# Optimization experiments

Hardware: AMD Instinct MI355X
Metric: run time of the kernel (lower is better)

Reference implementation:

```python
import jax, jax.numpy as jnp
import numpy as np

EMB_DIM = 2048
N_HEADS = 32
N_KV_HEADS = 8
HEAD_DIM = EMB_DIM // N_HEADS  # 64
N_REP = N_HEADS // N_KV_HEADS  # 4
B = 1
T = 2048


def setup_inputs() -> dict:
    key = jax.random.key(0)
    ks = jax.random.split(key, 7)
    x = jax.random.normal(ks[0], (B, T, EMB_DIM), dtype=jnp.float32)
    # RoPE tables, standard: cos/sin of shape (T, head_dim)
    inv_freq = 1.0 / (10000.0 ** (np.arange(0, HEAD_DIM, 2, dtype=np.float32) / HEAD_DIM))
    pos = np.arange(T, dtype=np.float32)
    ang = pos[:, None] * inv_freq[None, :]            # (T, head_dim/2)
    ang = np.concatenate([ang, ang], axis=-1)         # (T, head_dim)
    cos = jnp.asarray(np.cos(ang), dtype=jnp.float32)
    sin = jnp.asarray(np.sin(ang), dtype=jnp.float32)
    s = 0.02
    Wq = jax.random.normal(ks[1], (EMB_DIM, EMB_DIM), dtype=jnp.float32) * s
    Wk = jax.random.normal(ks[2], (N_KV_HEADS * HEAD_DIM, EMB_DIM), dtype=jnp.float32) * s
    Wv = jax.random.normal(ks[3], (N_KV_HEADS * HEAD_DIM, EMB_DIM), dtype=jnp.float32) * s
    Wo = jax.random.normal(ks[4], (EMB_DIM, EMB_DIM), dtype=jnp.float32) * s
    return {"x": x, "cos": cos, "sin": sin, "Wq": Wq, "Wk": Wk, "Wv": Wv, "Wo": Wo}


def apply_rope(t, cos, sin):
    # t: (b, h, T, d); cos/sin: (T, d)
    d = t.shape[-1]
    x1, x2 = t[..., : d // 2], t[..., d // 2:]
    rotated = jnp.concatenate([-x2, x1], axis=-1)
    return t * cos[None, None] + rotated * sin[None, None]


def reference(x, cos, sin, Wq, Wk, Wv, Wo):
    b, n_tok, _ = x.shape
    q = (x @ Wq.T).reshape(b, n_tok, N_HEADS, HEAD_DIM).transpose(0, 2, 1, 3)
    k = (x @ Wk.T).reshape(b, n_tok, N_KV_HEADS, HEAD_DIM).transpose(0, 2, 1, 3)
    v = (x @ Wv.T).reshape(b, n_tok, N_KV_HEADS, HEAD_DIM).transpose(0, 2, 1, 3)
    q = apply_rope(q, cos, sin)
    k = apply_rope(k, cos, sin)
    # repeat_interleave KV heads to n_heads
    k = jnp.repeat(k, N_REP, axis=1)
    v = jnp.repeat(v, N_REP, axis=1)
    scores = jnp.einsum("bhqd,bhkd->bhqk", q, k) / jnp.sqrt(jnp.float32(HEAD_DIM))
    causal = jnp.tril(jnp.ones((n_tok, n_tok), dtype=bool))
    scores = jnp.where(causal[None, None], scores, -jnp.inf)
    weights = jax.nn.softmax(scores, axis=-1)
    ctx = jnp.einsum("bhqk,bhkd->bhqd", weights, v)
    ctx = ctx.transpose(0, 2, 1, 3).reshape(b, n_tok, EMB_DIM)
    return ctx @ Wo.T
```

## Files before the change

### kernel.cpp

```cpp
#include <hip/hip_runtime.h>
#include <hip/hip_bf16.h>
#include <stdint.h>

#define EMB   2048
#define TOK   2048
#define NH    32
#define NKV   8
#define HD    64
#define QKVN  3072

typedef __attribute__((ext_vector_type(8))) short bf16x8;
typedef __attribute__((ext_vector_type(4))) float f32x4;
typedef __attribute__((ext_vector_type(16))) float f32x16;
typedef __attribute__((ext_vector_type(4))) unsigned int u32x4;

__device__ __forceinline__ void gld16(const void* g, void* l) {
  auto gp = reinterpret_cast<const int __attribute__((address_space(1)))*>(
      reinterpret_cast<uintptr_t>(g));
  auto lp = reinterpret_cast<int __attribute__((address_space(3)))*>(
      reinterpret_cast<uintptr_t>(l));
  __builtin_amdgcn_global_load_lds(gp, lp, 16, 0, 0);
}

__device__ __forceinline__ unsigned int cvtpk_bf16(float lo, float hi) {
  unsigned int r;
  asm("v_cvt_pk_bf16_f32 %0, %1, %2" : "=v"(r) : "v"(lo), "v"(hi));
  return r;
}
__device__ __forceinline__ void pl32swap(unsigned int &a, unsigned int &b) {
  asm volatile("v_permlane32_swap_b32 %0, %1" : "+v"(a), "+v"(b));
}
__device__ __forceinline__ float fexp2(float x) {
  float r;
  asm("v_exp_f32 %0, %1" : "=v"(r) : "v"(x));
  return r;
}

__global__ void cast_all(const float* __restrict__ x,  const float* __restrict__ wq,
                         const float* __restrict__ wk, const float* __restrict__ wv,
                         const float* __restrict__ wo,
                         __hip_bfloat16* __restrict__ xb,
                         __hip_bfloat16* __restrict__ wc,
                         __hip_bfloat16* __restrict__ wob) {
  const size_t M4 = (size_t)4 * 1024 * 1024;
  const size_t M1 = (size_t)1024 * 1024;
  size_t i = ((size_t)blockIdx.x * 256 + threadIdx.x) * 4;
  const float* src;
  __hip_bfloat16* dst;
  if (i < M4)                    { src = x  + i;                 dst = xb  + i; }
  else if (i < 2*M4)             { src = wq + (i - M4);          dst = wc  + (i - M4); }
  else if (i < 2*M4 + M1)        { src = wk + (i - 2*M4);        dst = wc  + M4 + (i - 2*M4); }
  else if (i < 2*M4 + 2*M1)      { src = wv + (i - 2*M4 - M1);   dst = wc  + M4 + M1 + (i - 2*M4 - M1); }
  else                           { src = wo + (i - 2*M4 - 2*M1); dst = wob + (i - 2*M4 - 2*M1); }
  float4 v = *reinterpret_cast<const float4*>(src);
  dst[0] = __float2bfloat16(v.x);
  dst[1] = __float2bfloat16(v.y);
  dst[2] = __float2bfloat16(v.z);
  dst[3] = __float2bfloat16(v.w);
}

__global__ __launch_bounds__(256) void gemm_bt(const __hip_bfloat16* __restrict__ A,
                                               const __hip_bfloat16* __restrict__ B,
                                               float* __restrict__ C,
                                               int M, int N, int K) {
  __shared__ __hip_bfloat16 As[2][128 * 64];
  __shared__ __hip_bfloat16 Bs[2][128 * 64];
  const int nbc = N >> 7;
  const int br  = blockIdx.x / nbc;
  const int bc  = blockIdx.x % nbc;
  const int tid  = threadIdx.x;
  const int lane = tid & 63;
  const int w    = tid >> 6;
  const int wr   = w >> 1, wc = w & 1;
  const int l15  = lane & 15;
  const int fk   = (lane >> 4) << 3;

  f32x4 acc[4][4];
#pragma unroll
  for (int m = 0; m < 4; ++m)
#pragma unroll
    for (int n = 0; n < 4; ++n) acc[m][n] = (f32x4){0.f, 0.f, 0.f, 0.f};

  const __hip_bfloat16* Ag = A + (size_t)br * 128 * K;
  const __hip_bfloat16* Bg = B + (size_t)bc * 128 * K;

  int srow[4], scol[4];
#pragma unroll
  for (int r = 0; r < 4; ++r) {
    int o = (w * 4 + r) * 1024 + lane * 16;
    srow[r] = o >> 7;
    scol[r] = (o & 127) >> 1;
  }

  auto stage = [&](int buf, int kt) {
#pragma unroll
    for (int r = 0; r < 4; ++r) {
      const int c = w * 4 + r;
      gld16(Ag + (size_t)srow[r] * K + kt + scol[r], (char*)As + buf * 16384 + c * 1024);
      gld16(Bg + (size_t)srow[r] * K + kt + scol[r], (char*)Bs + buf * 16384 + c * 1024);
    }
  };
  auto compute = [&](int buf) {
    bf16x8 a[4][2], b[4][2];
#pragma unroll
    for (int m = 0; m < 4; ++m)
#pragma unroll
      for (int kk = 0; kk < 2; ++kk)
        a[m][kk] = *reinterpret_cast<const bf16x8*>(
            (const char*)As + buf * 16384 + ((wr * 64 + m * 16 + l15) * 64 + kk * 32 + fk) * 2);
#pragma unroll
    for (int n = 0; n < 4; ++n)
#pragma unroll
      for (int kk = 0; kk < 2; ++kk)
        b[n][kk] = *reinterpret_cast<const bf16x8*>(
            (const char*)Bs + buf * 16384 + ((wc * 64 + n * 16 + l15) * 64 + kk * 32 + fk) * 2);
#pragma unroll
    for (int m = 0; m < 4; ++m)
#pragma unroll
      for (int n = 0; n < 4; ++n)
#pragma unroll
        for (int kk = 0; kk < 2; ++kk)
          acc[m][n] = __builtin_amdgcn_mfma_f32_16x16x32_bf16(a[m][kk], b[n][kk],
                                                              acc[m][n], 0, 0, 0);
  };

  stage(0, 0);
  __syncthreads();
  int cur = 0;
  int kt = 0;
  for (; kt < K - 64; kt += 64) {
    stage(cur ^ 1, kt + 64);
    compute(cur);
    __syncthreads();
    cur ^= 1;
  }
  compute(cur);

  const int row0 = br * 128 + wr * 64;
  const int col0 = bc * 128 + wc * 64;
  const int rb   = (lane >> 4) * 4;
#pragma unroll
  for (int m = 0; m < 4; ++m)
#pragma unroll
    for (int n = 0; n < 4; ++n)
#pragma unroll
      for (int r = 0; r < 4; ++r)
        C[(size_t)(row0 + m * 16 + rb + r) * N + col0 + n * 16 + l15] = acc[m][n][r];
}

#define QSCALE 0.1803368801111243f

__device__ __forceinline__ size_t kq_idx(int tile_row, int t, int d) {
  return ((size_t)tile_row) * 2048 +
         ((((d >> 4) * 64) + (((d >> 3) & 1) * 32) + (t & 31)) << 3) + (d & 7);
}

__global__ void rope_cast(const float* __restrict__ qkv,
                          const float* __restrict__ cosT, const float* __restrict__ sinT,
                          __hip_bfloat16* __restrict__ Qf,
                          __hip_bfloat16* __restrict__ Kf,
                          __hip_bfloat16* __restrict__ Vf) {
  const int QP = TOK * NH * (HD / 2);
  const int KP = TOK * NKV * (HD / 2);
  int idx = blockIdx.x * 256 + threadIdx.x;
  if (idx < QP) {
    int d = idx & 31, h = (idx >> 5) & 31, t = idx >> 10;
    const float* row = qkv + (size_t)t * QKVN + h * 64;
    float x1 = row[d], x2 = row[d + 32];
    float o1 = (x1 * cosT[t * 64 + d]      - x2 * sinT[t * 64 + d])      * QSCALE;
    float o2 = (x2 * cosT[t * 64 + d + 32] + x1 * sinT[t * 64 + d + 32]) * QSCALE;
    const int tile_row = h * 64 + (t >> 5);
    Qf[kq_idx(tile_row, t, d)]      = __float2bfloat16(o1);
    Qf[kq_idx(tile_row, t, d + 32)] = __float2bfloat16(o2);
  } else if (idx < QP + KP) {
    int j = idx - QP;
    int d = j & 31, hk = (j >> 5) & 7, t = j >> 8;
    const float* row = qkv + (size_t)t * QKVN + 2048 + hk * 64;
    float x1 = row[d], x2 = row[d + 32];
    float o1 = x1 * cosT[t * 64 + d]      - x2 * sinT[t * 64 + d];
    float o2 = x2 * cosT[t * 64 + d + 32] + x1 * sinT[t * 64 + d + 32];
    const int tile_row = hk * 64 + (t >> 5);
    Kf[kq_idx(tile_row, t, d)]      = __float2bfloat16(o1);
    Kf[kq_idx(tile_row, t, d + 32)] = __float2bfloat16(o2);
  } else {
    int vj = idx - QP - KP;
    int d = vj & 63, t = (vj >> 6) & (TOK - 1), hk = vj >> 17;
    float v = qkv[(size_t)t * QKVN + 2560 + hk * 64 + d];
    const size_t tb = ((size_t)hk * 64 + (t >> 5)) * 2048;
    const int c = (((t >> 4) & 1) * 128) + ((d >> 5) * 64) + (((t >> 3) & 1) * 32) + (d & 31);
    Vf[tb + (c << 3) + (t & 7)] = __float2bfloat16(v);
  }
}

struct KVb { bf16x8 k0, k1, k2, k3, v00, v01, v10, v11; };

__device__ __forceinline__ void load_kv(KVb& b, const __hip_bfloat16* Kt,
                                        const __hip_bfloat16* Vt, int tile,
                                        int lane) {
  const __hip_bfloat16* Kp = Kt + (size_t)tile * 2048 + lane * 8;
  b.k0 = *reinterpret_cast<const bf16x8*>(Kp);
  b.k1 = *reinterpret_cast<const bf16x8*>(Kp + 512);
  b.k2 = *reinterpret_cast<const bf16x8*>(Kp + 1024);
  b.k3 = *reinterpret_cast<const bf16x8*>(Kp + 1536);
  const __hip_bfloat16* Vp = Vt + (size_t)tile * 2048 + lane * 8;
  b.v00 = *reinterpret_cast<const bf16x8*>(Vp);
  b.v10 = *reinterpret_cast<const bf16x8*>(Vp + 512);
  b.v01 = *reinterpret_cast<const bf16x8*>(Vp + 1024);
  b.v11 = *reinterpret_cast<const bf16x8*>(Vp + 1536);
}

__device__ __forceinline__ void compute_tile(const KVb& b, bool diag,
                                             const bf16x8 (&qf)[4],
                                             int l31, int hi,
                                             float& m, float& l,
                                             f32x16& oa0, f32x16& oa1) {
  f32x16 st;
#pragma unroll
  for (int r = 0; r < 16; ++r) st[r] = 0.f;
  st = __builtin_amdgcn_mfma_f32_32x32x16_bf16(b.k0, qf[0], st, 0, 0, 0);
  st = __builtin_amdgcn_mfma_f32_32x32x16_bf16(b.k1, qf[1], st, 0, 0, 0);
  st = __builtin_amdgcn_mfma_f32_32x32x16_bf16(b.k2, qf[2], st, 0, 0, 0);
  st = __builtin_amdgcn_mfma_f32_32x32x16_bf16(b.k3, qf[3], st, 0, 0, 0);

  float s[16];
#pragma unroll
  for (int r = 0; r < 16; ++r) s[r] = st[r];
  if (diag) {
#pragma unroll
    for (int r = 0; r < 16; ++r) {
      const int crow = (r & 3) + 8 * (r >> 2) + 4 * hi;
      s[r] = (crow <= l31) ? s[r] : -1e30f;
    }
  }
  float t0 = fmaxf(fmaxf(s[0], s[1]),   fmaxf(s[2], s[3]));
  float t1 = fmaxf(fmaxf(s[4], s[5]),   fmaxf(s[6], s[7]));
  float t2 = fmaxf(fmaxf(s[8], s[9]),   fmaxf(s[10], s[11]));
  float t3 = fmaxf(fmaxf(s[12], s[13]), fmaxf(s[14], s[15]));
  float rmax = fmaxf(fmaxf(t0, t1), fmaxf(t2, t3));
  rmax = fmaxf(rmax, __shfl_xor(rmax, 32));

  const int allskip = __all(rmax <= m + 8.0f);
  const float mnew = allskip ? m : fmaxf(m, rmax);
  float p[16];
#pragma unroll
  for (int r = 0; r < 16; ++r) p[r] = fexp2(s[r] - mnew);
  float u0 = (p[0] + p[1]) + (p[2] + p[3]);
  float u1 = (p[4] + p[5]) + (p[6] + p[7]);
  float u2 = (p[8] + p[9]) + (p[10] + p[11]);
  float u3 = (p[12] + p[13]) + (p[14] + p[15]);
  float rsum = (u0 + u1) + (u2 + u3);
  rsum += __shfl_xor(rsum, 32);
  if (!allskip) {
    const float resc = fexp2(m - mnew);
    l *= resc;
    m = mnew;
#pragma unroll
    for (int r = 0; r < 16; ++r) { oa0[r] *= resc; oa1[r] *= resc; }
  }
  l += rsum;

  unsigned int wpk[8];
#pragma unroll
  for (int j = 0; j < 8; ++j) wpk[j] = cvtpk_bf16(p[2 * j], p[2 * j + 1]);

  {
    unsigned int a0 = wpk[0], b0 = wpk[2];  pl32swap(a0, b0);
    unsigned int a1 = wpk[1], b1 = wpk[3];  pl32swap(a1, b1);
    u32x4 pw; pw[0] = a0; pw[1] = a1; pw[2] = b0; pw[3] = b1;
    bf16x8 pf = *reinterpret_cast<bf16x8*>(&pw);
    oa0 = __builtin_amdgcn_mfma_f32_32x32x16_bf16(b.v00, pf, oa0, 0, 0, 0);
    oa1 = __builtin_amdgcn_mfma_f32_32x32x16_bf16(b.v10, pf, oa1, 0, 0, 0);
  }
  {
    unsigned int a0 = wpk[4], b0 = wpk[6];  pl32swap(a0, b0);
    unsigned int a1 = wpk[5], b1 = wpk[7];  pl32swap(a1, b1);
    u32x4 pw; pw[0] = a0; pw[1] = a1; pw[2] = b0; pw[3] = b1;
    bf16x8 pf = *reinterpret_cast<bf16x8*>(&pw);
    oa0 = __builtin_amdgcn_mfma_f32_32x32x16_bf16(b.v01, pf, oa0, 0, 0, 0);
    oa1 = __builtin_amdgcn_mfma_f32_32x32x16_bf16(b.v11, pf, oa1, 0, 0, 0);
  }
}

__global__ __launch_bounds__(256) void attn4(const __hip_bfloat16* __restrict__ Qf,
                                             const __hip_bfloat16* __restrict__ Kf,
                                             const __hip_bfloat16* __restrict__ Vf,
                                             __hip_bfloat16* __restrict__ ctx) {
  const int h     = blockIdx.x & 31;
  const int strip = 63 - (blockIdx.x >> 5);
  const int hk    = h >> 2;
  const int tid   = threadIdx.x;
  const int w     = tid >> 6;
  const int lane  = tid & 63;
  const int l31   = lane & 31, hi = lane >> 5;
  const int q0    = strip * 32;
  const int nt    = strip + 1;

  __shared__ float part[4][64][33];
  __shared__ float mlb[4][2][32];

  const __hip_bfloat16* Kt = Kf + (size_t)hk * 64 * 2048;
  const __hip_bfloat16* Vt = Vf + (size_t)hk * 64 * 2048;

  const __hip_bfloat16* Qp = Qf + ((size_t)h * 64 + strip) * 2048 + lane * 8;
  bf16x8 qf[4];
#pragma unroll
  for (int ks = 0; ks < 4; ++ks)
    qf[ks] = *reinterpret_cast<const bf16x8*>(Qp + ks * 512);

  f32x16 oa0, oa1;
#pragma unroll
  for (int r = 0; r < 16; ++r) { oa0[r] = 0.f; oa1[r] = 0.f; }
  float m = -1e30f, l = 0.f;

  if (w < nt) {
    KVb A, B;
    load_kv(A, Kt, Vt, w, lane);
    int t = w;
    for (;;) {
      int nx = t + 4;
      if (nx < nt) load_kv(B, Kt, Vt, nx, lane);
      compute_tile(A, t == nt - 1, qf, l31, hi, m, l, oa0, oa1);
      t = nx;
      if (t >= nt) break;
      nx = t + 4;
      if (nx < nt) load_kv(A, Kt, Vt, nx, lane);
      compute_tile(B, t == nt - 1, qf, l31, hi, m, l, oa0, oa1);
      t = nx;
      if (t >= nt) break;
    }
  }

#pragma unroll
  for (int r = 0; r < 16; ++r) {
    const int d = (r & 3) + 8 * (r >> 2) + 4 * hi;
    part[w][d][l31]      = oa0[r];
    part[w][d + 32][l31] = oa1[r];
  }
  if (hi == 0) { mlb[w][0][l31] = m; mlb[w][1][l31] = l; }
  __syncthreads();

  const int d  = tid & 63;
  const int qg = tid >> 6;
#pragma unroll
  for (int qq = 0; qq < 8; ++qq) {
    const int q = qg * 8 + qq;
    const float m0 = mlb[0][0][q], m1 = mlb[1][0][q];
    const float m2 = mlb[2][0][q], m3 = mlb[3][0][q];
    const float M = fmaxf(fmaxf(m0, m1), fmaxf(m2, m3));
    const float s0 = fexp2(m0 - M), s1 = fexp2(m1 - M);
    const float s2 = fexp2(m2 - M), s3 = fexp2(m3 - M);
    const float L = mlb[0][1][q] * s0 + mlb[1][1][q] * s1 +
                    mlb[2][1][q] * s2 + mlb[3][1][q] * s3;
    const float val = part[0][d][q] * s0 + part[1][d][q] * s1 +
                      part[2][d][q] * s2 + part[3][d][q] * s3;
    ctx[(size_t)(q0 + q) * EMB + h * HD + d] = __float2bfloat16(val / L);
  }
}

extern "C" void kernel_launch(void* const* d_in, const int* in_sizes, int n_in,
                              void* d_out, int out_size, void* d_ws, size_t ws_size,
                              hipStream_t stream) {
  const float* x    = (const float*)d_in[0];
  const float* cosT = (const float*)d_in[1];
  const float* sinT = (const float*)d_in[2];
  const float* Wq   = (const float*)d_in[3];
  const float* Wk   = (const float*)d_in[4];
  const float* Wv   = (const float*)d_in[5];
  const float* Wo   = (const float*)d_in[6];
  float* out = (float*)d_out;

  const size_t M4 = (size_t)4 * 1024 * 1024;
  const size_t M1 = (size_t)1024 * 1024;

  char* ws = (char*)d_ws;
  __hip_bfloat16* xb   = (__hip_bfloat16*)ws;
  __hip_bfloat16* Wc   = xb + M4;
  __hip_bfloat16* Wob  = Wc + (size_t)6 * M1;
  float*          qkv  = (float*)(Wob + M4);
  __hip_bfloat16* Qf   = (__hip_bfloat16*)(qkv + (size_t)TOK * QKVN);
  __hip_bfloat16* Kf   = Qf + (size_t)NH * TOK * HD;
  __hip_bfloat16* Vf   = Kf + (size_t)NKV * TOK * HD;
  __hip_bfloat16* ctxb = Vf + (size_t)NKV * HD * TOK;

  cast_all<<<14336, 256, 0, stream>>>(x, Wq, Wk, Wv, Wo, xb, Wc, Wob);

  gemm_bt<<<16 * 24, 256, 0, stream>>>(xb, Wc, qkv, TOK, QKVN, EMB);

  rope_cast<<<14336, 256, 0, stream>>>(qkv, cosT, sinT, Qf, Kf, Vf);

  attn4<<<64 * 32, 256, 0, stream>>>(Qf, Kf, Vf, ctxb);

  gemm_bt<<<16 * 16, 256, 0, stream>>>(ctxb, Wob, out, TOK, EMB, EMB);
}
```

Baseline: 146.0 us.

## Rewrite projection GEMM as 256x128 8-wave kernel with triple-buffered LDS

Replaces the 128x128 double-buffered GEMM with a 512-thread kernel computing 256x128 tiles. It uses a three-slot LDS ring that prefetches two K-steps ahead, an XOR-swizzled LDS layout to reduce bank conflicts, and an XCD-aware block remap. The kernel splits each K-step into two MFMA phases with explicit barriers, waitcnt and setprio so loads overlap compute. The cost is fewer blocks (192 and 128, under one wave on 256 CUs) and 144KB of dynamic LDS per block.

```diff
diff --git a/kernel.cpp b/kernel.cpp
--- a/kernel.cpp
+++ b/kernel.cpp
@@ -59,93 +59,139 @@
   dst[3] = __float2bfloat16(v.w);
 }
 
-__global__ __launch_bounds__(256) void gemm_bt(const __hip_bfloat16* __restrict__ A,
-                                               const __hip_bfloat16* __restrict__ B,
-                                               float* __restrict__ C,
-                                               int M, int N, int K) {
-  __shared__ __hip_bfloat16 As[2][128 * 64];
-  __shared__ __hip_bfloat16 Bs[2][128 * 64];
+#define SLOT_BYTES (48 * 1024)
+#define B_OFF      (32 * 1024)
+
+__global__ __launch_bounds__(512) void gemm8(const __hip_bfloat16* __restrict__ A,
+                                             const __hip_bfloat16* __restrict__ B,
+                                             float* __restrict__ C,
+                                             int M, int N, int K) {
+  extern __shared__ char lds[];
   const int nbc = N >> 7;
-  const int br  = blockIdx.x / nbc;
-  const int bc  = blockIdx.x % nbc;
+  const int nwg = gridDim.x;
+  int bid = blockIdx.x;
+  bid = (bid & 7) * (nwg >> 3) + (bid >> 3);
+  const int br = bid / nbc, bc = bid % nbc;
+
   const int tid  = threadIdx.x;
+  const int w    = tid >> 6;
   const int lane = tid & 63;
-  const int w    = tid >> 6;
-  const int wr   = w >> 1, wc = w & 1;
-  const int l15  = lane & 15;
-  const int fk   = (lane >> 4) << 3;
-
-  f32x4 acc[4][4];
-#pragma unroll
-  for (int m = 0; m < 4; ++m)
-#pragma unroll
-    for (int n = 0; n < 4; ++n) acc[m][n] = (f32x4){0.f, 0.f, 0.f, 0.f};
-
-  const __hip_bfloat16* Ag = A + (size_t)br * 128 * K;
+  const int wr   = w >> 2, wc = w & 3;
+  const int l15  = lane & 15, lg = lane >> 4;
+  const int swz  = (l15 & 4) << 3;
+
+  const __hip_bfloat16* Ag = A + (size_t)br * 256 * K;
   const __hip_bfloat16* Bg = B + (size_t)bc * 128 * K;
 
-  int srow[4], scol[4];
-#pragma unroll
-  for (int r = 0; r < 4; ++r) {
-    int o = (w * 4 + r) * 1024 + lane * 16;
-    srow[r] = o >> 7;
-    scol[r] = (o & 127) >> 1;
-  }
-
-  auto stage = [&](int buf, int kt) {
-#pragma unroll
-    for (int r = 0; r < 4; ++r) {
-      const int c = w * 4 + r;
-      gld16(Ag + (size_t)srow[r] * K + kt + scol[r], (char*)As + buf * 16384 + c * 1024);
-      gld16(Bg + (size_t)srow[r] * K + kt + scol[r], (char*)Bs + buf * 16384 + c * 1024);
+  const int srow = lane >> 3;
+  const int scol = ((lane & 7) * 8) ^ ((lane & 32) ? 16 : 0);
+
+  auto stage_unit = [&](const __hip_bfloat16* src, char* dst_base) {
+#pragma unroll
+    for (int i = 0; i < 2; ++i) {
+      const int chunk = w * 2 + i;
+      gld16(src + (size_t)(chunk * 8 + srow) * K + scol, dst_base + chunk * 1024);
     }
   };
-  auto compute = [&](int buf) {
-    bf16x8 a[4][2], b[4][2];
+
+  f32x4 acc[8][2];
+#pragma unroll
+  for (int m = 0; m < 8; ++m)
+#pragma unroll
+    for (int n = 0; n < 2; ++n) acc[m][n] = (f32x4){0.f, 0.f, 0.f, 0.f};
+
+  const int nt = K >> 6;
+
+  {
+    char* s0 = lds;
+    char* s1 = lds + SLOT_BYTES;
+    stage_unit(Ag,                    s0);
+    stage_unit(Ag + (size_t)128 * K,  s0 + 16384);
+    stage_unit(Bg,                    s0 + B_OFF);
+    stage_unit(Ag + 64,               s1);
+    stage_unit(Ag + (size_t)128 * K + 64, s1 + 16384);
+    stage_unit(Bg + 64,               s1 + B_OFF);
+  }
+  asm volatile("s_waitcnt vmcnt(6)" ::: "memory");
+  __builtin_amdgcn_s_barrier();
+
+  int slc = 0, sls = 2;
+  for (int t = 0; t < nt; ++t) {
+    const char* sa = lds + slc * SLOT_BYTES;
+    const char* sb = sa + B_OFF;
+    char* stg = lds + sls * SLOT_BYTES;
+    const int kt2 = (t + 2) * 64;
+    const bool do_stage = (t + 2) < nt;
+
+    bf16x8 afr[4][2], bfr[2][2];
 #pragma unroll
     for (int m = 0; m < 4; ++m)
 #pragma unroll
       for (int kk = 0; kk < 2; ++kk)
-        a[m][kk] = *reinterpret_cast<const bf16x8*>(
-            (const char*)As + buf * 16384 + ((wr * 64 + m * 16 + l15) * 64 + kk * 32 + fk) * 2);
-#pragma unroll
-    for (int n = 0; n < 4; ++n)
+        afr[m][kk] = *reinterpret_cast<const bf16x8*>(
+            sa + (((wr * 128 + m * 16 + l15) * 128 + kk * 64 + lg * 16) ^ swz));
+#pragma unroll
+    for (int n = 0; n < 2; ++n)
 #pragma unroll
       for (int kk = 0; kk < 2; ++kk)
-        b[n][kk] = *reinterpret_cast<const bf16x8*>(
-            (const char*)Bs + buf * 16384 + ((wc * 64 + n * 16 + l15) * 64 + kk * 32 + fk) * 2);
+        bfr[n][kk] = *reinterpret_cast<const bf16x8*>(
+            sb + (((wc * 32 + n * 16 + l15) * 128 + kk * 64 + lg * 16) ^ swz));
+    if (do_stage) {
+      stage_unit(Ag + kt2,                   stg);
+      stage_unit(Ag + (size_t)128 * K + kt2, stg + 16384);
+    }
+    __builtin_amdgcn_s_barrier();
+    asm volatile("s_waitcnt lgkmcnt(0)" ::: "memory");
+    __builtin_amdgcn_sched_barrier(0);
+    __builtin_amdgcn_s_setprio(1);
 #pragma unroll
     for (int m = 0; m < 4; ++m)
 #pragma unroll
-      for (int n = 0; n < 4; ++n)
+      for (int n = 0; n < 2; ++n)
 #pragma unroll
         for (int kk = 0; kk < 2; ++kk)
-          acc[m][n] = __builtin_amdgcn_mfma_f32_16x16x32_bf16(a[m][kk], b[n][kk],
+          acc[m][n] = __builtin_amdgcn_mfma_f32_16x16x32_bf16(afr[m][kk], bfr[n][kk],
                                                               acc[m][n], 0, 0, 0);
-  };
-
-  stage(0, 0);
-  __syncthreads();
-  int cur = 0;
-  int kt = 0;
-  for (; kt < K - 64; kt += 64) {
-    stage(cur ^ 1, kt + 64);
-    compute(cur);
-    __syncthreads();
-    cur ^= 1;
-  }
-  compute(cur);
-
-  const int row0 = br * 128 + wr * 64;
-  const int col0 = bc * 128 + wc * 64;
-  const int rb   = (lane >> 4) * 4;
-#pragma unroll
-  for (int m = 0; m < 4; ++m)
-#pragma unroll
-    for (int n = 0; n < 4; ++n)
+    __builtin_amdgcn_s_setprio(0);
+    __builtin_amdgcn_s_barrier();
+
+#pragma unroll
+    for (int m = 0; m < 4; ++m)
+#pragma unroll
+      for (int kk = 0; kk < 2; ++kk)
+        afr[m][kk] = *reinterpret_cast<const bf16x8*>(
+            sa + (((wr * 128 + 64 + m * 16 + l15) * 128 + kk * 64 + lg * 16) ^ swz));
+    if (do_stage) stage_unit(Bg + kt2, stg + B_OFF);
+    __builtin_amdgcn_s_barrier();
+    asm volatile("s_waitcnt lgkmcnt(0)" ::: "memory");
+    __builtin_amdgcn_sched_barrier(0);
+    __builtin_amdgcn_s_setprio(1);
+#pragma unroll
+    for (int m = 0; m < 4; ++m)
+#pragma unroll
+      for (int n = 0; n < 2; ++n)
+#pragma unroll
+        for (int kk = 0; kk < 2; ++kk)
+          acc[4 + m][n] = __builtin_amdgcn_mfma_f32_16x16x32_bf16(afr[m][kk], bfr[n][kk],
+                                                                  acc[4 + m][n], 0, 0, 0);
+    __builtin_amdgcn_s_setprio(0);
+    if (t < nt - 2) asm volatile("s_waitcnt vmcnt(6)" ::: "memory");
+    else            asm volatile("s_waitcnt vmcnt(0)" ::: "memory");
+    __builtin_amdgcn_s_barrier();
+
+    slc = (slc == 2) ? 0 : slc + 1;
+    sls = (sls == 2) ? 0 : sls + 1;
+  }
+
+  const int row0 = br * 256 + wr * 128;
+  const int col0 = bc * 128 + wc * 32;
+#pragma unroll
+  for (int m = 0; m < 8; ++m)
+#pragma unroll
+    for (int n = 0; n < 2; ++n)
 #pragma unroll
       for (int r = 0; r < 4; ++r)
-        C[(size_t)(row0 + m * 16 + rb + r) * N + col0 + n * 16 + l15] = acc[m][n][r];
+        C[(size_t)(row0 + m * 16 + lg * 4 + r) * N + col0 + n * 16 + l15] = acc[m][n][r];
 }
 
 #define QSCALE 0.1803368801111243f
@@ -382,13 +428,16 @@
   __hip_bfloat16* Vf   = Kf + (size_t)NKV * TOK * HD;
   __hip_bfloat16* ctxb = Vf + (size_t)NKV * HD * TOK;
 
+  hipFuncSetAttribute(reinterpret_cast<const void*>(gemm8),
+                      hipFuncAttributeMaxDynamicSharedMemorySize, 3 * SLOT_BYTES);
+
   cast_all<<<14336, 256, 0, stream>>>(x, Wq, Wk, Wv, Wo, xb, Wc, Wob);
 
-  gemm_bt<<<16 * 24, 256, 0, stream>>>(xb, Wc, qkv, TOK, QKVN, EMB);
+  gemm8<<<192, 512, 3 * SLOT_BYTES, stream>>>(xb, Wc, qkv, TOK, QKVN, EMB);
 
   rope_cast<<<14336, 256, 0, stream>>>(qkv, cosT, sinT, Qf, Kf, Vf);
 
   attn4<<<64 * 32, 256, 0, stream>>>(Qf, Kf, Vf, ctxb);
 
-  gemm_bt<<<16 * 16, 256, 0, stream>>>(ctxb, Wob, out, TOK, EMB, EMB);
-}
+  gemm8<<<128, 512, 3 * SLOT_BYTES, stream>>>(ctxb, Wob, out, TOK, EMB, EMB);
+}
```

New measurement: 157.0 us. 1.08x slower.
